# Kernel tuning notes

Hardware: AMD Instinct MI355X
Metric: run time of the kernel (lower is better)

The kernel has to match this reference:

```python
import jax, jax.numpy as jnp
import numpy as np

N_HEADS = 8
NUM_GROUPS = 2
HEAD_DIM = 256
ROPE_DIM = 64
IDIM = 2048
GROUP_SIZE = N_HEADS // NUM_GROUPS  # 4
ODIM = N_HEADS * HEAD_DIM           # 2048
N_KV = NUM_GROUPS * HEAD_DIM        # 512
EPS = 1e-6


def rms_norm(x, gamma):
    # normalize over last dim (head_dim)
    var = jnp.mean(jnp.square(x), axis=-1, keepdims=True)
    return x * jax.lax.rsqrt(var + EPS) * gamma


def rotate_half(x):
    x1, x2 = jnp.split(x, 2, axis=-1)
    return jnp.concatenate([-x2, x1], axis=-1)


def apply_rope(x, cos, sin):
    # x: (..., L, rope_dim); cos/sin: (L, rope_dim) broadcast
    return x * cos + rotate_half(x) * sin


def setup_inputs() -> dict:
    key = jax.random.key(0)
    ks = jax.random.split(key, 10)
    B, L = 1, 4096
    x = jax.random.normal(ks[0], (B, L, IDIM), dtype=jnp.float32)
    # rope angles
    inv_freq = 1.0 / (10000.0 ** (jnp.arange(0, ROPE_DIM, 2, dtype=jnp.float32) / ROPE_DIM))
    t = jnp.arange(L, dtype=jnp.float32)
    freqs = jnp.outer(t, inv_freq)                      # (L, rope_dim/2)
    emb = jnp.concatenate([freqs, freqs], axis=-1)      # (L, rope_dim)
    cos = jnp.cos(emb)
    sin = jnp.sin(emb)
    # causal mask: True = masked out
    mask = jnp.triu(jnp.ones((L, L), dtype=bool), k=1)
    s = 0.02
    wq = jax.random.normal(ks[1], (IDIM, ODIM * 2), dtype=jnp.float32) * s
    wk = jax.random.normal(ks[2], (IDIM, N_KV), dtype=jnp.float32) * s
    wv = jax.random.normal(ks[3], (IDIM, N_KV), dtype=jnp.float32) * s
    wo = jax.random.normal(ks[4], (ODIM, IDIM), dtype=jnp.float32) * s
    q_gamma = jnp.ones((HEAD_DIM,), dtype=jnp.float32)
    k_gamma = jnp.ones((HEAD_DIM,), dtype=jnp.float32)
    return {"x": x, "cos": cos, "sin": sin, "mask": mask,
            "wq": wq, "wk": wk, "wv": wv, "wo": wo,
            "q_gamma": q_gamma, "k_gamma": k_gamma}


def reference(x, cos, sin, mask, wq, wk, wv, wo, q_gamma, k_gamma):
    b, L, _ = x.shape
    scale = HEAD_DIM ** -0.5
    # query + output gate
    q_raw = (x @ wq).reshape(b, L, N_HEADS, 2 * HEAD_DIM)
    q, gate = jnp.split(q_raw, 2, axis=-1)
    gate = gate.reshape(b, L, ODIM)
    q = jnp.transpose(q, (0, 2, 1, 3))                  # (b, h, L, d)
    # grouped K/V
    k = (x @ wk).reshape(b, L, NUM_GROUPS, HEAD_DIM).transpose(0, 2, 1, 3)  # (b, g, L, d)
    v = (x @ wv).reshape(b, L, NUM_GROUPS, HEAD_DIM).transpose(0, 2, 1, 3)
    # QK RMSNorm
    q = rms_norm(q, q_gamma)
    k = rms_norm(k, k_gamma)
    # partial RoPE on first ROPE_DIM dims
    q = jnp.concatenate([apply_rope(q[..., :ROPE_DIM], cos, sin), q[..., ROPE_DIM:]], axis=-1)
    k = jnp.concatenate([apply_rope(k[..., :ROPE_DIM], cos, sin), k[..., ROPE_DIM:]], axis=-1)
    # GQA without materializing repeated K/V: head h = g*GROUP_SIZE + s
    qg = q.reshape(b, NUM_GROUPS, GROUP_SIZE, L, HEAD_DIM)
    dots = jnp.einsum('bgsid,bgjd->bgsij', qg, k) * scale
    dots = jnp.where(mask, -jnp.inf, dots)
    attn = jax.nn.softmax(dots, axis=-1)
    out = jnp.einsum('bgsij,bgjd->bgsid', attn, v)      # (b, g, gs, L, d)
    out = out.reshape(b, N_HEADS, L, HEAD_DIM).transpose(0, 2, 1, 3).reshape(b, L, ODIM)
    out = out * jax.nn.sigmoid(gate)
    return out @ wo
```

## Files before the change

### kernel.cpp

```cpp
#include <hip/hip_runtime.h>
#include <hip/hip_bf16.h>
#include <math.h>

typedef __bf16 bf16_t;
typedef __bf16 bf16x4 __attribute__((ext_vector_type(4)));
typedef __bf16 bf16x8 __attribute__((ext_vector_type(8)));
typedef float  f32x4  __attribute__((ext_vector_type(4)));
typedef float  f32x16 __attribute__((ext_vector_type(16)));
typedef unsigned int u32x4 __attribute__((ext_vector_type(4)));

typedef const __attribute__((address_space(1))) void* gas_ptr;
typedef __attribute__((address_space(3))) void* las_ptr;

#define RD_ 64

__global__ __launch_bounds__(256) void cvt_f32_bf16(const float* __restrict__ in,
                                                    bf16_t* __restrict__ out) {
  int i = (blockIdx.x * 256 + threadIdx.x) * 4;
  float4 v = *(const float4*)&in[i];
  bf16x4 w;
  w[0] = (bf16_t)v.x; w[1] = (bf16_t)v.y; w[2] = (bf16_t)v.z; w[3] = (bf16_t)v.w;
  *(bf16x4*)&out[i] = w;
}

__global__ __launch_bounds__(256) void transpose_cvt(const float* __restrict__ in,
                                                     bf16_t* __restrict__ out,
                                                     int R, int C) {
  __shared__ bf16_t t[32][33];
  int tx = threadIdx.x & 31, ty = threadIdx.x >> 5;
  int c0 = blockIdx.x * 32, r0 = blockIdx.y * 32;
#pragma unroll
  for (int i = 0; i < 4; i++)
    t[ty + 8 * i][tx] = (bf16_t)in[(size_t)(r0 + ty + 8 * i) * C + c0 + tx];
  __syncthreads();
#pragma unroll
  for (int i = 0; i < 4; i++)
    out[(size_t)(c0 + ty + 8 * i) * R + r0 + tx] = t[tx][ty + 8 * i];
}

__global__ __launch_bounds__(256) void transpose_bf16(const bf16_t* __restrict__ in,
                                                      bf16_t* __restrict__ out,
                                                      int R, int C) {
  __shared__ bf16_t t[32][33];
  int tx = threadIdx.x & 31, ty = threadIdx.x >> 5;
  int c0 = blockIdx.x * 32, r0 = blockIdx.y * 32;
#pragma unroll
  for (int i = 0; i < 4; i++)
    t[ty + 8 * i][tx] = in[(size_t)(r0 + ty + 8 * i) * C + c0 + tx];
  __syncthreads();
#pragma unroll
  for (int i = 0; i < 4; i++)
    out[(size_t)(c0 + ty + 8 * i) * R + r0 + tx] = t[tx][ty + 8 * i];
}

#define GM 128
#define GN 128
#define GK 32

template <typename OutT>
__global__ __launch_bounds__(256) void gemm_bt(const bf16_t* __restrict__ A,
                                               const bf16_t* __restrict__ Bt,
                                               OutT* __restrict__ C,
                                               int M, int N, int K) {
  __shared__ bf16_t As[GM * GK];
  __shared__ bf16_t Bs[GN * GK];
  int tid  = threadIdx.x;
  int lane = tid & 63, wave = tid >> 6;
  int wm = (wave & 1) * 64, wn = (wave >> 1) * 64;
  int bm = blockIdx.x * GM, bn = blockIdx.y * GN;
  int qd = lane >> 4, lr = lane & 15;

  f32x4 acc[4][4] = {};

  int srow = wave * 16 + (lane >> 2);
  int scol = (lane & 3) * 8;
  const bf16_t* ga0 = A  + (size_t)(bm + srow) * K + scol;
  const bf16_t* ga1 = A  + (size_t)(bm + 64 + srow) * K + scol;
  const bf16_t* gb0 = Bt + (size_t)(bn + srow) * K + scol;
  const bf16_t* gb1 = Bt + (size_t)(bn + 64 + srow) * K + scol;
  las_ptr lA0 = (las_ptr)(As + wave * 512);
  las_ptr lA1 = (las_ptr)(As + 64 * 32 + wave * 512);
  las_ptr lB0 = (las_ptr)(Bs + wave * 512);
  las_ptr lB1 = (las_ptr)(Bs + 64 * 32 + wave * 512);

  for (int k0 = 0; k0 < K; k0 += GK) {
    __syncthreads();
    __builtin_amdgcn_global_load_lds((gas_ptr)(ga0 + k0), lA0, 16, 0, 0);
    __builtin_amdgcn_global_load_lds((gas_ptr)(ga1 + k0), lA1, 16, 0, 0);
    __builtin_amdgcn_global_load_lds((gas_ptr)(gb0 + k0), lB0, 16, 0, 0);
    __builtin_amdgcn_global_load_lds((gas_ptr)(gb1 + k0), lB1, 16, 0, 0);
    __syncthreads();

    bf16x8 af[4], bfr[4];
#pragma unroll
    for (int t = 0; t < 4; t++) {
      af[t]  = *(const bf16x8*)&As[(wm + t * 16 + lr) * GK + qd * 8];
      bfr[t] = *(const bf16x8*)&Bs[(wn + t * 16 + lr) * GK + qd * 8];
    }
#pragma unroll
    for (int mt = 0; mt < 4; mt++)
#pragma unroll
      for (int nt = 0; nt < 4; nt++)
        acc[mt][nt] = __builtin_amdgcn_mfma_f32_16x16x32_bf16(af[mt], bfr[nt], acc[mt][nt], 0, 0, 0);
  }

#pragma unroll
  for (int mt = 0; mt < 4; mt++) {
    int rb = bm + wm + mt * 16 + qd * 4;
#pragma unroll
    for (int nt = 0; nt < 4; nt++) {
      int cc = bn + wn + nt * 16 + lr;
#pragma unroll
      for (int r = 0; r < 4; r++)
        C[(size_t)(rb + r) * N + cc] = (OutT)acc[mt][nt][r];
    }
  }
}

template <int NHEADS, int HSTRIDE>
__global__ __launch_bounds__(256) void norm_rope(const bf16_t* __restrict__ in,
                                                 bf16_t* __restrict__ out,
                                                 const float* __restrict__ cosv,
                                                 const float* __restrict__ sinv,
                                                 const float* __restrict__ gamma) {
  int lane = threadIdx.x & 63;
  int idx  = blockIdx.x * 4 + (threadIdx.x >> 6);
  int l = idx / NHEADS, h = idx % NHEADS;
  size_t base = (size_t)l * NHEADS * HSTRIDE + (size_t)h * HSTRIDE;
  int d0 = lane * 4;

  bf16x4 raw = *(const bf16x4*)&in[base + d0];
  float x[4];
#pragma unroll
  for (int i = 0; i < 4; i++) x[i] = (float)raw[i];
  float ss = x[0] * x[0] + x[1] * x[1] + x[2] * x[2] + x[3] * x[3];
#pragma unroll
  for (int off = 32; off >= 1; off >>= 1) ss += __shfl_xor(ss, off);
  float inv = 1.0f / sqrtf(ss * (1.0f / 256.0f) + 1e-6f);

  float4 gr = *(const float4*)&gamma[d0];
  float n[4];
#pragma unroll
  for (int i = 0; i < 4; i++) n[i] = x[i] * inv * ((const float*)&gr)[i];

  float p[4];
#pragma unroll
  for (int i = 0; i < 4; i++) p[i] = __shfl_xor(n[i], 8);
  float o[4];
#pragma unroll
  for (int i = 0; i < 4; i++) o[i] = n[i];
  if (lane < 16) {
    float4 cr = *(const float4*)&cosv[(size_t)l * RD_ + d0];
    float4 sr = *(const float4*)&sinv[(size_t)l * RD_ + d0];
#pragma unroll
    for (int i = 0; i < 4; i++) {
      float rh = (lane < 8) ? -p[i] : p[i];
      o[i] = n[i] * ((const float*)&cr)[i] + rh * ((const float*)&sr)[i];
    }
  }
  bf16x4 w;
#pragma unroll
  for (int i = 0; i < 4; i++) w[i] = (bf16_t)o[i];
  *(bf16x4*)&out[base + d0] = w;
}

__global__ __launch_bounds__(256, 2) void attn_mfma(const bf16_t* __restrict__ qraw,
                                                    const bf16_t* __restrict__ kn,
                                                    const bf16_t* __restrict__ vt,
                                                    bf16_t* __restrict__ outg) {
  __shared__ __align__(16) bf16_t ks[64 * 256];
  __shared__ __align__(16) bf16_t vs[256 * 64];
  int tid = threadIdx.x, lane = tid & 63, wave = tid >> 6;
  int qs = wave & 1, pj = wave >> 1;
  int m = lane & 31, hi = lane >> 5;
  int h = blockIdx.y, g = h >> 2;
  int qb = (h < 4) ? (63 - (int)blockIdx.x) : (int)blockIdx.x;
  int iw = qb * 64;
  int qrow0 = iw + qs * 32;
  int qg = qrow0 + m;
  int qmax = qrow0 + 31;

  bf16x8 qf[16];
  {
    const bf16_t* qp = qraw + (size_t)(qrow0 + m) * 4096 + h * 512 + hi * 8;
#pragma unroll
    for (int kb = 0; kb < 16; kb++) qf[kb] = *(const bf16x8*)(qp + kb * 16);
  }

  int jrow = pj * 32 + m;
  int xk = jrow & 7;
  const bf16_t* kb4[4];
#pragma unroll
  for (int b = 0; b < 4; b++)
    kb4[b] = ks + jrow * 256 + ((b ^ (xk >> 1)) * 2 + (hi ^ (xk & 1))) * 8;
  int xv = m & 7;
  const bf16_t* vb[2];
#pragma unroll
  for (int ks2 = 0; ks2 < 2; ks2++)
    vb[ks2] = vs + m * 64 + (((pj * 4 + ks2 * 2 + hi) ^ xv) * 8);

  int krow0 = wave * 2 + hi;
  int kg = m ^ (krow0 & 7);
  const bf16_t* ksrc = kn + (size_t)krow0 * 512 + g * 256 + kg * 8;
  int vd0 = wave * 8 + (lane >> 3);
  int vg = (lane & 7) ^ ((lane >> 3) & 7);
  const bf16_t* vsrc = vt + (size_t)(g * 256 + vd0) * 4096 + vg * 8;

  f32x16 o[8] = {};
  float ladd = 0.0f;

  int nit = qb + 1;
  for (int it = 0; it < nit; it++) {
    __syncthreads();
    const bf16_t* kp = ksrc + (size_t)it * 32768;
    const bf16_t* vp = vsrc + (size_t)it * 64;
#pragma unroll
    for (int s = 0; s < 8; s++)
      __builtin_amdgcn_global_load_lds((gas_ptr)(kp + s * 4096),
                                       (las_ptr)(ks + (s * 4 + wave) * 512), 16, 0, 0);
#pragma unroll
    for (int s = 0; s < 8; s++)
      __builtin_amdgcn_global_load_lds((gas_ptr)(vp + (size_t)s * 131072),
                                       (las_ptr)(vs + (s * 4 + wave) * 512), 16, 0, 0);
    __syncthreads();

    int j0w = it * 64 + pj * 32;
    if (j0w > qmax) continue;

    f32x16 sa = {};
#pragma unroll
    for (int kb = 0; kb < 16; kb++) {
      bf16x8 kf = *(const bf16x8*)(kb4[kb & 3] + (kb >> 2) * 64);
      sa = __builtin_amdgcn_mfma_f32_32x32x16_bf16(kf, qf[kb], sa, 0, 0, 0);
    }

    bool diag = (j0w + 31 > qrow0);
#pragma unroll
    for (int ks2 = 0; ks2 < 2; ks2++) {
      float pp[8];
#pragma unroll
      for (int r = 0; r < 8; r++) {
        int rr = ks2 * 8 + r;
        float e = __expf(sa[rr] * 0.0625f - 20.0f);
        if (diag) {
          int jr = j0w + (rr & 3) + 8 * (rr >> 2) + 4 * hi;
          if (jr > qg) e = 0.0f;
        }
        pp[r] = e;
      }
      unsigned a0, b0, a1, b1;
      asm("v_cvt_pk_bf16_f32 %0, %1, %2" : "=v"(a0) : "v"(pp[0]), "v"(pp[1]));
      asm("v_cvt_pk_bf16_f32 %0, %1, %2" : "=v"(b0) : "v"(pp[4]), "v"(pp[5]));
      asm("v_cvt_pk_bf16_f32 %0, %1, %2" : "=v"(a1) : "v"(pp[2]), "v"(pp[3]));
      asm("v_cvt_pk_bf16_f32 %0, %1, %2" : "=v"(b1) : "v"(pp[6]), "v"(pp[7]));
      asm("v_permlane32_swap_b32 %0, %1" : "+v"(a0), "+v"(b0));
      asm("v_permlane32_swap_b32 %0, %1" : "+v"(a1), "+v"(b1));
      u32x4 uw = {a0, a1, b0, b1};
      bf16x8 pa = __builtin_bit_cast(bf16x8, uw);
#pragma unroll
      for (int i = 0; i < 4; i++) {
        unsigned w = uw[i];
        ladd += __builtin_bit_cast(float, w << 16);
        ladd += __builtin_bit_cast(float, w & 0xffff0000u);
      }
#pragma unroll
      for (int dt = 0; dt < 8; dt++) {
        bf16x8 vf = *(const bf16x8*)(vb[ks2] + dt * 2048);
        o[dt] = __builtin_amdgcn_mfma_f32_32x32x16_bf16(pa, vf, o[dt], 0, 0, 0);
      }
    }
  }

  __syncthreads();
  float* lbuf = (float*)vs;
  lbuf[wave * 64 + lane] = ladd;
  float* ob = (float*)ks + qs * 4096;
  if (pj == 1) {
#pragma unroll
    for (int dt = 0; dt < 4; dt++)
#pragma unroll
      for (int r = 0; r < 16; r++)
        ob[(dt * 16 + r) * 64 + lane] = o[dt][r];
  }
  __syncthreads();
  float linv[16];
  const bf16_t* gb = qraw + (size_t)qrow0 * 4096 + h * 512 + 256;
  if (pj == 0) {
    float lt = lbuf[qs * 64 + lane] + lbuf[qs * 64 + (lane ^ 32)]
             + lbuf[(2 + qs) * 64 + lane] + lbuf[(2 + qs) * 64 + (lane ^ 32)];
#pragma unroll
    for (int r = 0; r < 16; r++)
      linv[r] = 1.0f / __shfl(lt, (r & 3) + 8 * (r >> 2) + 4 * hi, 64);
#pragma unroll
    for (int dt = 0; dt < 4; dt++)
#pragma unroll
      for (int r = 0; r < 16; r++) {
        float val = o[dt][r] + ob[(dt * 16 + r) * 64 + lane];
        int q = (r & 3) + 8 * (r >> 2) + 4 * hi;
        int d = dt * 32 + m;
        float gt = (float)gb[(size_t)q * 4096 + d];
        float sg = 1.0f / (1.0f + __expf(-gt));
        outg[(size_t)(qrow0 + q) * 2048 + h * 256 + d] = (bf16_t)(val * linv[r] * sg);
      }
  }
  __syncthreads();
  if (pj == 1) {
#pragma unroll
    for (int dt = 4; dt < 8; dt++)
#pragma unroll
      for (int r = 0; r < 16; r++)
        ob[((dt - 4) * 16 + r) * 64 + lane] = o[dt][r];
  }
  __syncthreads();
  if (pj == 0) {
#pragma unroll
    for (int dt = 4; dt < 8; dt++)
#pragma unroll
      for (int r = 0; r < 16; r++) {
        float val = o[dt][r] + ob[((dt - 4) * 16 + r) * 64 + lane];
        int q = (r & 3) + 8 * (r >> 2) + 4 * hi;
        int d = dt * 32 + m;
        float gt = (float)gb[(size_t)q * 4096 + d];
        float sg = 1.0f / (1.0f + __expf(-gt));
        outg[(size_t)(qrow0 + q) * 2048 + h * 256 + d] = (bf16_t)(val * linv[r] * sg);
      }
  }
}

extern "C" void kernel_launch(void* const* d_in, const int* in_sizes, int n_in,
                              void* d_out, int out_size, void* d_ws, size_t ws_size,
                              hipStream_t stream) {
  const float* x    = (const float*)d_in[0];
  const float* cosv = (const float*)d_in[1];
  const float* sinv = (const float*)d_in[2];
  const float* wq   = (const float*)d_in[4];
  const float* wk   = (const float*)d_in[5];
  const float* wv   = (const float*)d_in[6];
  const float* wo   = (const float*)d_in[7];
  const float* qg   = (const float*)d_in[8];
  const float* kg   = (const float*)d_in[9];
  float* outp = (float*)d_out;

  char* ws = (char*)d_ws;
  size_t off = 0;
  auto alloc = [&](size_t bytes) { char* p = ws + off; off += (bytes + 255) & ~255ull; return p; };

  bf16_t* x_bf  = (bf16_t*)alloc((size_t)4096 * 2048 * 2);
  bf16_t* wqT   = (bf16_t*)alloc((size_t)2048 * 4096 * 2);
  bf16_t* wkT   = (bf16_t*)alloc((size_t)2048 * 512 * 2);
  bf16_t* wvT   = (bf16_t*)alloc((size_t)2048 * 512 * 2);
  bf16_t* woT   = (bf16_t*)alloc((size_t)2048 * 2048 * 2);
  bf16_t* q_raw = (bf16_t*)alloc((size_t)4096 * 4096 * 2);
  bf16_t* k_raw = (bf16_t*)alloc((size_t)4096 * 512 * 2);
  bf16_t* v_b   = (bf16_t*)alloc((size_t)4096 * 512 * 2);
  bf16_t* v_t   = (bf16_t*)alloc((size_t)512 * 4096 * 2);
  bf16_t* attn_g= (bf16_t*)alloc((size_t)4096 * 2048 * 2);

  dim3 blk(256);
  cvt_f32_bf16<<<8192, blk, 0, stream>>>(x, x_bf);

  transpose_cvt<<<dim3(4096 / 32, 2048 / 32), blk, 0, stream>>>(wq, wqT, 2048, 4096);
  transpose_cvt<<<dim3(512 / 32, 2048 / 32), blk, 0, stream>>>(wk, wkT, 2048, 512);
  transpose_cvt<<<dim3(512 / 32, 2048 / 32), blk, 0, stream>>>(wv, wvT, 2048, 512);
  transpose_cvt<<<dim3(2048 / 32, 2048 / 32), blk, 0, stream>>>(wo, woT, 2048, 2048);

  gemm_bt<bf16_t><<<dim3(4096 / 128, 4096 / 128), blk, 0, stream>>>(x_bf, wqT, q_raw, 4096, 4096, 2048);
  gemm_bt<bf16_t><<<dim3(4096 / 128, 512 / 128), blk, 0, stream>>>(x_bf, wkT, k_raw, 4096, 512, 2048);
  gemm_bt<bf16_t><<<dim3(4096 / 128, 512 / 128), blk, 0, stream>>>(x_bf, wvT, v_b, 4096, 512, 2048);

  norm_rope<8, 512><<<4096 * 8 / 4, blk, 0, stream>>>(q_raw, q_raw, cosv, sinv, qg);
  norm_rope<2, 256><<<4096 * 2 / 4, blk, 0, stream>>>(k_raw, k_raw, cosv, sinv, kg);

  transpose_bf16<<<dim3(512 / 32, 4096 / 32), blk, 0, stream>>>(v_b, v_t, 4096, 512);

  attn_mfma<<<dim3(64, 8), blk, 0, stream>>>(q_raw, k_raw, v_t, attn_g);

  gemm_bt<float><<<dim3(4096 / 128, 2048 / 128), blk, 0, stream>>>(attn_g, woT, outp, 4096, 2048, 2048);
}
```

Measured before the change: 604.4 us.

## Split causal attention KV range across blocks with partial outputs and combine kernel

Each attention block now handles 128 query rows, with the KV range split into chunks of up to 32 tiles. This gives 640 blocks with balanced work instead of 512 uneven causal blocks. K/V staging is double-buffered so the next tile loads while the current one computes. Partial O and row sums are written to fp32 scratch, and a new combine kernel sums them and applies normalization and the sigmoid gate. The cost is extra global traffic for the fp32 partials and one additional launch.

```diff
diff --git a/kernel.cpp b/kernel.cpp
--- a/kernel.cpp
+++ b/kernel.cpp
@@ -167,16 +167,22 @@
 __global__ __launch_bounds__(256, 2) void attn_mfma(const bf16_t* __restrict__ qraw,
                                                     const bf16_t* __restrict__ kn,
                                                     const bf16_t* __restrict__ vt,
-                                                    bf16_t* __restrict__ outg) {
-  __shared__ __align__(16) bf16_t ks[64 * 256];
-  __shared__ __align__(16) bf16_t vs[256 * 64];
+                                                    float* __restrict__ pO,
+                                                    float* __restrict__ pL) {
+  __shared__ __align__(16) bf16_t ks[2][32 * 256];
+  __shared__ __align__(16) bf16_t vs[2][256 * 32];
   int tid = threadIdx.x, lane = tid & 63, wave = tid >> 6;
-  int qs = wave & 1, pj = wave >> 1;
   int m = lane & 31, hi = lane >> 5;
   int h = blockIdx.y, g = h >> 2;
-  int qb = (h < 4) ? (63 - (int)blockIdx.x) : (int)blockIdx.x;
-  int iw = qb * 64;
-  int qrow0 = iw + qs * 32;
+
+  int x = 79 - (int)blockIdx.x;
+  int qb = 0, acc0 = 0;
+  for (;;) { int nc = (qb >> 3) + 1; if (acc0 + nc > x) break; acc0 += nc; qb++; }
+  int c = x - acc0;
+  int tile0 = c * 32;
+  int nt = 4 * qb + 4 - tile0; if (nt > 32) nt = 32;
+
+  int qrow0 = qb * 128 + wave * 32;
   int qg = qrow0 + m;
   int qmax = qrow0 + 31;
 
@@ -187,143 +193,149 @@
     for (int kb = 0; kb < 16; kb++) qf[kb] = *(const bf16x8*)(qp + kb * 16);
   }
 
-  int jrow = pj * 32 + m;
-  int xk = jrow & 7;
-  const bf16_t* kb4[4];
+  int xk = m & 7;
+  int kofs[4];
 #pragma unroll
   for (int b = 0; b < 4; b++)
-    kb4[b] = ks + jrow * 256 + ((b ^ (xk >> 1)) * 2 + (hi ^ (xk & 1))) * 8;
-  int xv = m & 7;
-  const bf16_t* vb[2];
-#pragma unroll
-  for (int ks2 = 0; ks2 < 2; ks2++)
-    vb[ks2] = vs + m * 64 + (((pj * 4 + ks2 * 2 + hi) ^ xv) * 8);
-
-  int krow0 = wave * 2 + hi;
-  int kg = m ^ (krow0 & 7);
-  const bf16_t* ksrc = kn + (size_t)krow0 * 512 + g * 256 + kg * 8;
-  int vd0 = wave * 8 + (lane >> 3);
-  int vg = (lane & 7) ^ ((lane >> 3) & 7);
-  const bf16_t* vsrc = vt + (size_t)(g * 256 + vd0) * 4096 + vg * 8;
+    kofs[b] = m * 256 + ((b ^ (xk >> 1)) * 2 + (hi ^ (xk & 1))) * 8;
+  int swv = (m ^ (m >> 2)) & 3;
+  int vofs[2];
+#pragma unroll
+  for (int k2 = 0; k2 < 2; k2++)
+    vofs[k2] = m * 32 + (((k2 * 2 + hi) ^ swv) * 8);
+
+  const bf16_t* ksrc = kn + (size_t)(wave * 2 + hi) * 512 + g * 256
+                          + (size_t)((m ^ ((wave * 2 + hi) & 7)) * 8);
+  int swsrc = ((lane >> 2) ^ (lane >> 4)) & 3;
+  const bf16_t* vsrc = vt + (size_t)(g * 256 + wave * 16 + (lane >> 2)) * 4096
+                          + (size_t)(((lane & 3) ^ swsrc) * 8);
 
   f32x16 o[8] = {};
   float ladd = 0.0f;
 
-  int nit = qb + 1;
-  for (int it = 0; it < nit; it++) {
+  bf16x8 onesf;
+
+#define STAGE(buf, j0)                                                                  \
+  do {                                                                                  \
+    bf16_t* kd = &ks[buf][0] + wave * 512;                                              \
+    bf16_t* vd = &vs[buf][0] + wave * 512;                                              \
+    _Pragma("unroll")                                                                   \
+    for (int s = 0; s < 4; s++)                                                         \
+      __builtin_amdgcn_global_load_lds((gas_ptr)(ksrc + (size_t)(j0) * 512 + s * 4096), \
+                                       (las_ptr)(kd + s * 2048), 16, 0, 0);             \
+    _Pragma("unroll")                                                                   \
+    for (int s = 0; s < 4; s++)                                                         \
+      __builtin_amdgcn_global_load_lds((gas_ptr)(vsrc + (size_t)(j0) + (size_t)s * 262144), \
+                                       (las_ptr)(vd + s * 2048), 16, 0, 0);             \
+  } while (0)
+
+  STAGE(0, tile0 * 32);
+  asm volatile("s_waitcnt vmcnt(0)" ::: "memory");
+  __syncthreads();
+
+  for (int t = 0; t < nt; t++) {
+    int cur = t & 1;
+    if (t + 1 < nt) STAGE(cur ^ 1, (tile0 + t + 1) * 32);
+    int j0 = (tile0 + t) * 32;
+    if (j0 <= qmax) {
+      f32x16 sa = {};
+#pragma unroll
+      for (int kb = 0; kb < 16; kb++) {
+        bf16x8 kf = *(const bf16x8*)&ks[cur][kofs[kb & 3] + (kb >> 2) * 64];
+        sa = __builtin_amdgcn_mfma_f32_32x32x16_bf16(kf, qf[kb], sa, 0, 0, 0);
+      }
+
+      bool diag = (j0 + 31 > qrow0);
+#pragma unroll
+      for (int k2 = 0; k2 < 2; k2++) {
+        float pp[8];
+#pragma unroll
+        for (int r = 0; r < 8; r++) {
+          int rr = k2 * 8 + r;
+          float e = __expf(sa[rr] * 0.0625f - 20.0f);
+          if (diag) {
+            int jr = j0 + (rr & 3) + 8 * (rr >> 2) + 4 * hi;
+            if (jr > qg) e = 0.0f;
+          }
+          pp[r] = e;
+        }
+        unsigned a0, b0, a1, b1;
+        asm("v_cvt_pk_bf16_f32 %0, %1, %2" : "=v"(a0) : "v"(pp[0]), "v"(pp[1]));
+        asm("v_cvt_pk_bf16_f32 %0, %1, %2" : "=v"(b0) : "v"(pp[4]), "v"(pp[5]));
+        asm("v_cvt_pk_bf16_f32 %0, %1, %2" : "=v"(a1) : "v"(pp[2]), "v"(pp[3]));
+        asm("v_cvt_pk_bf16_f32 %0, %1, %2" : "=v"(b1) : "v"(pp[6]), "v"(pp[7]));
+        asm("v_permlane32_swap_b32 %0, %1" : "+v"(a0), "+v"(b0));
+        asm("v_permlane32_swap_b32 %0, %1" : "+v"(a1), "+v"(b1));
+        u32x4 uw = {a0, a1, b0, b1};
+        bf16x8 pa = __builtin_bit_cast(bf16x8, uw);
+#pragma unroll
+        for (int i = 0; i < 4; i++) {
+          unsigned w = uw[i];
+          ladd += __builtin_bit_cast(float, w << 16);
+          ladd += __builtin_bit_cast(float, w & 0xffff0000u);
+        }
+#pragma unroll
+        for (int dt = 0; dt < 8; dt++) {
+          bf16x8 vf = *(const bf16x8*)&vs[cur][vofs[k2] + dt * 1024];
+          o[dt] = __builtin_amdgcn_mfma_f32_32x32x16_bf16(pa, vf, o[dt], 0, 0, 0);
+        }
+      }
+    }
+    asm volatile("s_waitcnt vmcnt(0)" ::: "memory");
     __syncthreads();
-    const bf16_t* kp = ksrc + (size_t)it * 32768;
-    const bf16_t* vp = vsrc + (size_t)it * 64;
-#pragma unroll
-    for (int s = 0; s < 8; s++)
-      __builtin_amdgcn_global_load_lds((gas_ptr)(kp + s * 4096),
-                                       (las_ptr)(ks + (s * 4 + wave) * 512), 16, 0, 0);
-#pragma unroll
-    for (int s = 0; s < 8; s++)
-      __builtin_amdgcn_global_load_lds((gas_ptr)(vp + (size_t)s * 131072),
-                                       (las_ptr)(vs + (s * 4 + wave) * 512), 16, 0, 0);
-    __syncthreads();
-
-    int j0w = it * 64 + pj * 32;
-    if (j0w > qmax) continue;
-
-    f32x16 sa = {};
-#pragma unroll
-    for (int kb = 0; kb < 16; kb++) {
-      bf16x8 kf = *(const bf16x8*)(kb4[kb & 3] + (kb >> 2) * 64);
-      sa = __builtin_amdgcn_mfma_f32_32x32x16_bf16(kf, qf[kb], sa, 0, 0, 0);
-    }
-
-    bool diag = (j0w + 31 > qrow0);
-#pragma unroll
-    for (int ks2 = 0; ks2 < 2; ks2++) {
-      float pp[8];
-#pragma unroll
-      for (int r = 0; r < 8; r++) {
-        int rr = ks2 * 8 + r;
-        float e = __expf(sa[rr] * 0.0625f - 20.0f);
-        if (diag) {
-          int jr = j0w + (rr & 3) + 8 * (rr >> 2) + 4 * hi;
-          if (jr > qg) e = 0.0f;
-        }
-        pp[r] = e;
-      }
-      unsigned a0, b0, a1, b1;
-      asm("v_cvt_pk_bf16_f32 %0, %1, %2" : "=v"(a0) : "v"(pp[0]), "v"(pp[1]));
-      asm("v_cvt_pk_bf16_f32 %0, %1, %2" : "=v"(b0) : "v"(pp[4]), "v"(pp[5]));
-      asm("v_cvt_pk_bf16_f32 %0, %1, %2" : "=v"(a1) : "v"(pp[2]), "v"(pp[3]));
-      asm("v_cvt_pk_bf16_f32 %0, %1, %2" : "=v"(b1) : "v"(pp[6]), "v"(pp[7]));
-      asm("v_permlane32_swap_b32 %0, %1" : "+v"(a0), "+v"(b0));
-      asm("v_permlane32_swap_b32 %0, %1" : "+v"(a1), "+v"(b1));
-      u32x4 uw = {a0, a1, b0, b1};
-      bf16x8 pa = __builtin_bit_cast(bf16x8, uw);
-#pragma unroll
-      for (int i = 0; i < 4; i++) {
-        unsigned w = uw[i];
-        ladd += __builtin_bit_cast(float, w << 16);
-        ladd += __builtin_bit_cast(float, w & 0xffff0000u);
-      }
-#pragma unroll
-      for (int dt = 0; dt < 8; dt++) {
-        bf16x8 vf = *(const bf16x8*)(vb[ks2] + dt * 2048);
-        o[dt] = __builtin_amdgcn_mfma_f32_32x32x16_bf16(pa, vf, o[dt], 0, 0, 0);
-      }
-    }
-  }
-
-  __syncthreads();
-  float* lbuf = (float*)vs;
-  lbuf[wave * 64 + lane] = ladd;
-  float* ob = (float*)ks + qs * 4096;
-  if (pj == 1) {
-#pragma unroll
-    for (int dt = 0; dt < 4; dt++)
-#pragma unroll
-      for (int r = 0; r < 16; r++)
-        ob[(dt * 16 + r) * 64 + lane] = o[dt][r];
-  }
-  __syncthreads();
-  float linv[16];
-  const bf16_t* gb = qraw + (size_t)qrow0 * 4096 + h * 512 + 256;
-  if (pj == 0) {
-    float lt = lbuf[qs * 64 + lane] + lbuf[qs * 64 + (lane ^ 32)]
-             + lbuf[(2 + qs) * 64 + lane] + lbuf[(2 + qs) * 64 + (lane ^ 32)];
-#pragma unroll
-    for (int r = 0; r < 16; r++)
-      linv[r] = 1.0f / __shfl(lt, (r & 3) + 8 * (r >> 2) + 4 * hi, 64);
-#pragma unroll
-    for (int dt = 0; dt < 4; dt++)
-#pragma unroll
-      for (int r = 0; r < 16; r++) {
-        float val = o[dt][r] + ob[(dt * 16 + r) * 64 + lane];
-        int q = (r & 3) + 8 * (r >> 2) + 4 * hi;
-        int d = dt * 32 + m;
-        float gt = (float)gb[(size_t)q * 4096 + d];
-        float sg = 1.0f / (1.0f + __expf(-gt));
-        outg[(size_t)(qrow0 + q) * 2048 + h * 256 + d] = (bf16_t)(val * linv[r] * sg);
-      }
-  }
-  __syncthreads();
-  if (pj == 1) {
-#pragma unroll
-    for (int dt = 4; dt < 8; dt++)
-#pragma unroll
-      for (int r = 0; r < 16; r++)
-        ob[((dt - 4) * 16 + r) * 64 + lane] = o[dt][r];
-  }
-  __syncthreads();
-  if (pj == 0) {
-#pragma unroll
-    for (int dt = 4; dt < 8; dt++)
-#pragma unroll
-      for (int r = 0; r < 16; r++) {
-        float val = o[dt][r] + ob[((dt - 4) * 16 + r) * 64 + lane];
-        int q = (r & 3) + 8 * (r >> 2) + 4 * hi;
-        int d = dt * 32 + m;
-        float gt = (float)gb[(size_t)q * 4096 + d];
-        float sg = 1.0f / (1.0f + __expf(-gt));
-        outg[(size_t)(qrow0 + q) * 2048 + h * 256 + d] = (bf16_t)(val * linv[r] * sg);
-      }
+  }
+#undef STAGE
+
+  int slot = h * 80 + x;
+  float lo = ladd + __shfl_xor(ladd, 32);
+  if (hi == 0) pL[(size_t)slot * 128 + wave * 32 + m] = lo;
+  size_t ob = (size_t)slot * 32768 + (size_t)(wave * 32) * 256;
+#pragma unroll
+  for (int dt = 0; dt < 8; dt++)
+#pragma unroll
+    for (int r = 0; r < 16; r++) {
+      int q = (r & 3) + 8 * (r >> 2) + 4 * hi;
+      pO[ob + (size_t)q * 256 + dt * 32 + m] = o[dt][r];
+    }
+}
+
+__global__ __launch_bounds__(256) void attn_combine(const float* __restrict__ pO,
+                                                    const float* __restrict__ pL,
+                                                    const bf16_t* __restrict__ qraw,
+                                                    bf16_t* __restrict__ outg) {
+  int qb = blockIdx.x, h = blockIdx.y;
+  int g8 = qb >> 3, rr = qb & 7;
+  int off = qb + 4 * g8 * (g8 - 1) + rr * g8;
+  int nc = g8 + 1;
+  int tid = threadIdx.x;
+  int r = tid >> 1, half = tid & 1;
+  int row = qb * 128 + r;
+  size_t base = (size_t)(h * 80 + off);
+
+  float lsum = 0.0f;
+  for (int c = 0; c < nc; c++) lsum += pL[(base + c) * 128 + r];
+  float linv = 1.0f / lsum;
+
+  const bf16_t* gb = qraw + (size_t)row * 4096 + h * 512 + 256 + half * 128;
+  bf16_t* op = outg + (size_t)row * 2048 + h * 256 + half * 128;
+  size_t pbase = base * 32768 + (size_t)r * 256 + half * 128;
+#pragma unroll 4
+  for (int d = 0; d < 128; d += 4) {
+    float a0 = 0, a1 = 0, a2 = 0, a3 = 0;
+    for (int c = 0; c < nc; c++) {
+      float4 v = *(const float4*)&pO[pbase + (size_t)c * 32768 + d];
+      a0 += v.x; a1 += v.y; a2 += v.z; a3 += v.w;
+    }
+    float vv[4] = {a0, a1, a2, a3};
+    bf16x4 gr = *(const bf16x4*)&gb[d];
+    bf16x4 w;
+#pragma unroll
+    for (int i = 0; i < 4; i++) {
+      float gt = (float)gr[i];
+      float sg = 1.0f / (1.0f + __expf(-gt));
+      w[i] = (bf16_t)(vv[i] * linv * sg);
+    }
+    *(bf16x4*)&op[d] = w;
   }
 }
 
@@ -345,16 +357,23 @@
   size_t off = 0;
   auto alloc = [&](size_t bytes) { char* p = ws + off; off += (bytes + 255) & ~255ull; return p; };
 
-  bf16_t* x_bf  = (bf16_t*)alloc((size_t)4096 * 2048 * 2);
-  bf16_t* wqT   = (bf16_t*)alloc((size_t)2048 * 4096 * 2);
-  bf16_t* wkT   = (bf16_t*)alloc((size_t)2048 * 512 * 2);
-  bf16_t* wvT   = (bf16_t*)alloc((size_t)2048 * 512 * 2);
-  bf16_t* woT   = (bf16_t*)alloc((size_t)2048 * 2048 * 2);
-  bf16_t* q_raw = (bf16_t*)alloc((size_t)4096 * 4096 * 2);
-  bf16_t* k_raw = (bf16_t*)alloc((size_t)4096 * 512 * 2);
-  bf16_t* v_b   = (bf16_t*)alloc((size_t)4096 * 512 * 2);
-  bf16_t* v_t   = (bf16_t*)alloc((size_t)512 * 4096 * 2);
-  bf16_t* attn_g= (bf16_t*)alloc((size_t)4096 * 2048 * 2);
+  bf16_t* q_raw  = (bf16_t*)alloc((size_t)4096 * 4096 * 2);
+  bf16_t* k_raw  = (bf16_t*)alloc((size_t)4096 * 512 * 2);
+  bf16_t* v_t    = (bf16_t*)alloc((size_t)512 * 4096 * 2);
+  bf16_t* attn_g = (bf16_t*)alloc((size_t)4096 * 2048 * 2);
+  bf16_t* woT    = (bf16_t*)alloc((size_t)2048 * 2048 * 2);
+
+  size_t scratch0 = off;
+  bf16_t* x_bf = (bf16_t*)alloc((size_t)4096 * 2048 * 2);
+  bf16_t* wqT  = (bf16_t*)alloc((size_t)2048 * 4096 * 2);
+  bf16_t* wkT  = (bf16_t*)alloc((size_t)2048 * 512 * 2);
+  bf16_t* wvT  = (bf16_t*)alloc((size_t)2048 * 512 * 2);
+  bf16_t* v_b  = (bf16_t*)alloc((size_t)4096 * 512 * 2);
+
+  float* pO = (float*)(ws + scratch0);
+  size_t poEnd = scratch0 + (size_t)640 * 32768 * 4;
+  if (off < poEnd) off = (poEnd + 255) & ~255ull;
+  float* pL = (float*)alloc((size_t)640 * 128 * 4);
 
   dim3 blk(256);
   cvt_f32_bf16<<<8192, blk, 0, stream>>>(x, x_bf);
@@ -373,7 +392,8 @@
 
   transpose_bf16<<<dim3(512 / 32, 4096 / 32), blk, 0, stream>>>(v_b, v_t, 4096, 512);
 
-  attn_mfma<<<dim3(64, 8), blk, 0, stream>>>(q_raw, k_raw, v_t, attn_g);
+  attn_mfma<<<dim3(80, 8), blk, 0, stream>>>(q_raw, k_raw, v_t, pO, pL);
+  attn_combine<<<dim3(32, 8), blk, 0, stream>>>(pO, pL, q_raw, attn_g);
 
   gemm_bt<float><<<dim3(4096 / 128, 2048 / 128), blk, 0, stream>>>(attn_g, woT, outp, 4096, 2048, 2048);
 }
```

New measurement: 654.9 us. +8.4%, slower.
